# Kernel optimization log

Measured on AMD Instinct MI355X. Metric: run time of the kernel, lower is better.

Reference implementation:

```python
import jax, jax.numpy as jnp
import numpy as np

B, S, E, H, M, Q = 2, 2048, 768, 12, 768, 4
D = E // H  # head_dim = 64
EPS = 1e-5


def _layernorm(x, g, b):
    m = jnp.mean(x, axis=-1, keepdims=True)
    v = jnp.mean((x - m) ** 2, axis=-1, keepdims=True)
    return (x - m) / jnp.sqrt(v + EPS) * g + b


def setup_inputs() -> dict:
    key = jax.random.key(0)
    ks = jax.random.split(key, 12)
    w = lambda k, shape, s=0.02: (jax.random.normal(k, shape) * s).astype(jnp.float32)
    return {
        "x": jax.random.normal(ks[0], (B, S, E), dtype=jnp.float32),
        "ln1_g": jnp.ones((E,), jnp.float32), "ln1_b": jnp.zeros((E,), jnp.float32),
        "wq": w(ks[1], (E, E)), "bq": jnp.zeros((E,), jnp.float32),
        "wk": w(ks[2], (E, E)), "bk": jnp.zeros((E,), jnp.float32),
        "wv": w(ks[3], (E, E)), "bv": jnp.zeros((E,), jnp.float32),
        "wo": w(ks[4], (E, E)), "bo": jnp.zeros((E,), jnp.float32),
        "ln2_g": jnp.ones((E,), jnp.float32), "ln2_b": jnp.zeros((E,), jnp.float32),
        "w1": w(ks[5], (E, Q * M)), "b1": jnp.zeros((Q * M,), jnp.float32),
        "wvqc": w(ks[6], (M, M)), "bvqc": jnp.zeros((M,), jnp.float32),
        "w2": w(ks[7], (Q * M, E)), "b2": jnp.zeros((E,), jnp.float32),
    }


def reference(x, ln1_g, ln1_b, wq, bq, wk, bk, wv, bv, wo, bo,
              ln2_g, ln2_b, w1, b1, wvqc, bvqc, w2, b2):
    b, s, e = x.shape
    h, d = H, e // H

    # --- attention branch (pre-norm, per-query-L2-normalized logits) ---
    xn = _layernorm(x, ln1_g, ln1_b)
    q = (xn @ wq + bq).reshape(b, s, h, d).transpose(0, 2, 1, 3)  # bhsd
    k = (xn @ wk + bk).reshape(b, s, h, d).transpose(0, 2, 1, 3)
    v = (xn @ wv + bv).reshape(b, s, h, d).transpose(0, 2, 1, 3)

    qk = jnp.einsum('bhsd,bhtd->bhst', q, k)                       # [B,H,S,S]
    q_norm2 = jnp.clip(jnp.sum(q * q, axis=-1, keepdims=True), 1e-5)  # [B,H,S,1]
    logits = qk / jnp.sqrt(d * q_norm2)
    attn = jax.nn.softmax(logits, axis=-1)
    vals = jnp.einsum('bhst,bhtd->bhsd', attn, v)
    vals = vals.transpose(0, 2, 1, 3).reshape(b, s, e)
    x = x + (vals @ wo + bo)  # residual; attn dropout is identity in eval

    # --- quantum-style FeedForward with overlapping q_stride slices ---
    xn2 = _layernorm(x, ln2_g, ln2_b)
    hmid = xn2 @ w1 + b1                                           # [B,S,Q*M]
    m = wvqc.shape[0]
    qstride = w1.shape[1] // m
    # overlapping slices h[..., i:i+M] for i in 0..Q-1, stacked on a new axis
    sl = jnp.stack([hmid[..., i:i + m] for i in range(qstride)], axis=2)  # [B,S,Q,M]
    hv = sl @ wvqc + bvqc                                          # vqc linear
    hv = hv.transpose(0, 1, 3, 2).reshape(b, s, qstride * m)       # interleave
    hv = jax.nn.gelu(hv, approximate=False)
    out = x + (hv @ w2 + b2)
    return out
```

## Files before the change

kernel.cpp:

```cpp
#include <hip/hip_runtime.h>
#include <hip/hip_bf16.h>
#include <math.h>

typedef unsigned short ushort_t;
typedef __attribute__((ext_vector_type(8))) short short8;
typedef __attribute__((ext_vector_type(8))) __bf16 bf16x8;
typedef __attribute__((ext_vector_type(4))) float f32x4;
typedef __attribute__((ext_vector_type(4))) unsigned u32x4;

#define SDIM 2048
#define EDIM 768
#define NTOK 4096

static __device__ __forceinline__ ushort_t f2bf(float f) {
  unsigned u = __builtin_bit_cast(unsigned, f);
  u += 0x7fff + ((u >> 16) & 1);
  return (ushort_t)(u >> 16);
}
static __device__ __forceinline__ float bf2f(ushort_t h) {
  return __builtin_bit_cast(float, (unsigned)h << 16);
}
static __device__ __forceinline__ f32x4 mfma16(short8 a, short8 b, f32x4 c) {
  return __builtin_amdgcn_mfma_f32_16x16x32_bf16(
      __builtin_bit_cast(bf16x8, a), __builtin_bit_cast(bf16x8, b), c, 0, 0, 0);
}
static __device__ __forceinline__ void gload_lds16(const void* g, void* l) {
  __builtin_amdgcn_global_load_lds(
      (const __attribute__((address_space(1))) void*)g,
      (__attribute__((address_space(3))) void*)l, 16, 0, 0);
}
static __device__ __forceinline__ unsigned cvtpk(float lo, float hi) {
  unsigned r;
  asm("v_cvt_pk_bf16_f32 %0, %1, %2" : "=v"(r) : "v"(lo), "v"(hi));
  return r;
}

__global__ void k_castT5(const float* __restrict__ wq, const float* __restrict__ wk,
                         const float* __restrict__ wv, const float* __restrict__ wo,
                         const float* __restrict__ wvqc, ushort_t* __restrict__ oqkv,
                         ushort_t* __restrict__ owo, ushort_t* __restrict__ ovqc) {
  __shared__ float tile[32][33];
  const int z = blockIdx.z;
  const float* in = z == 0 ? wq : z == 1 ? wk : z == 2 ? wv : z == 3 ? wo : wvqc;
  ushort_t* out = z < 3 ? oqkv + (size_t)z * 768 * 768 : (z == 3 ? owo : ovqc);
  int c0 = blockIdx.x * 32, r0 = blockIdx.y * 32;
  int tx = threadIdx.x, ty = threadIdx.y;
#pragma unroll
  for (int i = 0; i < 32; i += 8)
    tile[ty + i][tx] = in[(size_t)(r0 + ty + i) * 768 + c0 + tx];
  __syncthreads();
#pragma unroll
  for (int i = 0; i < 32; i += 8)
    out[(size_t)(c0 + ty + i) * 768 + r0 + tx] = f2bf(tile[tx][ty + i]);
}

__global__ void k_castT(const float* __restrict__ in, ushort_t* __restrict__ out,
                        int R, int C) {
  __shared__ float tile[32][33];
  int c0 = blockIdx.x * 32, r0 = blockIdx.y * 32;
  int tx = threadIdx.x, ty = threadIdx.y;
#pragma unroll
  for (int i = 0; i < 32; i += 8)
    tile[ty + i][tx] = in[(size_t)(r0 + ty + i) * C + c0 + tx];
  __syncthreads();
#pragma unroll
  for (int i = 0; i < 32; i += 8)
    out[(size_t)(c0 + ty + i) * R + r0 + tx] = f2bf(tile[tx][ty + i]);
}

__global__ void k_vT(const ushort_t* __restrict__ in, ushort_t* __restrict__ out) {
  __shared__ ushort_t tile[32][34];
  int bh = blockIdx.z;
  int t0 = blockIdx.x * 32, d0 = blockIdx.y * 32;
  const ushort_t* ib = in + (size_t)bh * SDIM * 64;
  ushort_t* ob = out + (size_t)bh * 64 * SDIM;
  int tx = threadIdx.x, ty = threadIdx.y;
#pragma unroll
  for (int i = 0; i < 32; i += 8)
    tile[ty + i][tx] = ib[(size_t)(t0 + ty + i) * 64 + d0 + tx];
  __syncthreads();
  const int T = t0 + tx, tb = T & ~63, tl = T & 63;
  const int tperm =
      tb + 32 * (tl >> 5) + 8 * ((tl >> 2) & 3) + 4 * ((tl >> 4) & 1) + (tl & 3);
#pragma unroll
  for (int i = 0; i < 32; i += 8)
    ob[(size_t)(d0 + ty + i) * SDIM + tperm] = tile[tx][ty + i];
}

__global__ void k_w1shift(const float* __restrict__ w1, ushort_t* __restrict__ w1s) {
  int idx = blockIdx.x * 256 + threadIdx.x;
  int e = idx / 768, m = idx - (idx / 768) * 768;
#pragma unroll
  for (int i = 0; i < 4; i++)
    w1s[((size_t)i * 768 + e) * 768 + m] = f2bf(w1[(size_t)e * 3072 + i + m]);
}

__global__ __launch_bounds__(256) void k_b1eff(const float* __restrict__ b1,
                                               const ushort_t* __restrict__ wvqcT,
                                               const float* __restrict__ bvqc,
                                               float* __restrict__ b1e) {
  const int n = blockIdx.x;
  const int i = n & 3, j = n >> 2;
  const int t = threadIdx.x;
  float s = 0.f;
  for (int m = t; m < 768; m += 256)
    s += b1[i + m] * bf2f(wvqcT[(size_t)j * 768 + m]);
#pragma unroll
  for (int mm = 32; mm; mm >>= 1) s += __shfl_xor(s, mm);
  __shared__ float red[4];
  if ((t & 63) == 0) red[t >> 6] = s;
  __syncthreads();
  if (t == 0) b1e[n] = red[0] + red[1] + red[2] + red[3] + bvqc[j];
}

__global__ __launch_bounds__(256) void k_ln(const float* __restrict__ x,
                                            const float* __restrict__ gam,
                                            const float* __restrict__ bet,
                                            ushort_t* __restrict__ out) {
  const int row = blockIdx.x, t = threadIdx.x;
  const float* xr = x + (size_t)row * EDIM;
  float v0 = xr[t], v1 = xr[t + 256], v2 = xr[t + 512];
  float s = v0 + v1 + v2;
  float s2 = v0 * v0 + v1 * v1 + v2 * v2;
#pragma unroll
  for (int m = 32; m; m >>= 1) { s += __shfl_xor(s, m); s2 += __shfl_xor(s2, m); }
  __shared__ float red[8];
  const int wid = t >> 6, lane = t & 63;
  if (lane == 0) { red[wid] = s; red[4 + wid] = s2; }
  __syncthreads();
  s = red[0] + red[1] + red[2] + red[3];
  s2 = red[4] + red[5] + red[6] + red[7];
  float mean = s * (1.f / EDIM);
  float var = s2 * (1.f / EDIM) - mean * mean;
  float rstd = rsqrtf(var + 1e-5f);
  ushort_t* orow = out + (size_t)row * EDIM;
  orow[t] = f2bf((v0 - mean) * rstd * gam[t] + bet[t]);
  orow[t + 256] = f2bf((v1 - mean) * rstd * gam[t + 256] + bet[t + 256]);
  orow[t + 512] = f2bf((v2 - mean) * rstd * gam[t + 512] + bet[t + 512]);
}

__global__ __launch_bounds__(256) void k_qscale(const ushort_t* __restrict__ q,
                                                float* __restrict__ qs) {
  const int lane = threadIdx.x & 63, w = threadIdx.x >> 6;
  const int row = blockIdx.x * 4 + w;
  float v = bf2f(q[(size_t)row * 64 + lane]);
  float s = v * v;
#pragma unroll
  for (int m = 32; m; m >>= 1) s += __shfl_xor(s, m);
  if (lane == 0) qs[row] = rsqrtf(64.f * fmaxf(s, 1e-5f));
}

template <int MODE, int BM, int BN>
__global__ __launch_bounds__(256) void k_gemm(
    const ushort_t* __restrict__ A, const ushort_t* __restrict__ Bt, int lda,
    int ldb, int kc, const float* __restrict__ b0, const float* __restrict__ b1p,
    const float* __restrict__ b2p, float* __restrict__ outF,
    const float* __restrict__ resid, ushort_t* __restrict__ o0,
    ushort_t* __restrict__ o1, ushort_t* __restrict__ o2, int ldc) {
  constexpr int MT = BM / 32, NT = BN / 32;
  constexpr int NPA = BM / 32, NPB = BN / 32;
  __shared__ ushort_t As[2][BM * 64];
  __shared__ ushort_t Bs[2][BN * 64];
  const int t = threadIdx.x;
  const int m0 = blockIdx.x * BM, n0 = blockIdx.y * BN;
  if (MODE == 3) Bt += (size_t)blockIdx.z * 768 * 768;
  const int rowa = t >> 3;
  const int gseg = ((t & 7) ^ (rowa & 7)) * 8;
  const ushort_t* ga = A + (size_t)(m0 + rowa) * lda + gseg;
  const ushort_t* gb = Bt + (size_t)(n0 + rowa) * ldb + gseg;
  const int ldst = t * 8;
  const int lane = t & 63, wid = t >> 6;
  const int g = lane >> 4, c = lane & 15;
  const int wm = (wid >> 1) * (BM / 2), wn = (wid & 1) * (BN / 2);
  const int swz = (c & 7) * 8;
  f32x4 acc[MT][NT] = {};

#define STAGE(BUF, K0)                                                           \
  {                                                                              \
    _Pragma("unroll") for (int p = 0; p < NPA; p++)                              \
        gload_lds16(ga + (K0) + (size_t)(p * 32) * lda, As[BUF] + p * 2048 + ldst);\
    _Pragma("unroll") for (int p = 0; p < NPB; p++)                              \
        gload_lds16(gb + (K0) + (size_t)(p * 32) * ldb, Bs[BUF] + p * 2048 + ldst);\
  }

  STAGE(0, 0);
  __syncthreads();
  int cur = 0;
  for (int k0 = 0; k0 < kc; k0 += 64) {
    if (k0 + 64 < kc) STAGE(cur ^ 1, k0 + 64);
    short8 af[2][MT], bfr[2][NT];
#pragma unroll
    for (int kk = 0; kk < 2; kk++) {
#pragma unroll
      for (int mt = 0; mt < MT; mt++)
        af[kk][mt] = *(const short8*)(As[cur] + (wm + mt * 16 + c) * 64 +
                                      ((g * 8 + kk * 32) ^ swz));
#pragma unroll
      for (int nt = 0; nt < NT; nt++)
        bfr[kk][nt] = *(const short8*)(Bs[cur] + (wn + nt * 16 + c) * 64 +
                                       ((g * 8 + kk * 32) ^ swz));
    }
    __builtin_amdgcn_s_setprio(1);
#pragma unroll
    for (int kk = 0; kk < 2; kk++)
#pragma unroll
      for (int mt = 0; mt < MT; mt++)
#pragma unroll
        for (int nt = 0; nt < NT; nt++)
          acc[mt][nt] = mfma16(af[kk][mt], bfr[kk][nt], acc[mt][nt]);
    __builtin_amdgcn_s_setprio(0);
    __syncthreads();
    cur ^= 1;
  }
#undef STAGE

#pragma unroll
  for (int mt = 0; mt < MT; mt++) {
#pragma unroll
    for (int nt = 0; nt < NT; nt++) {
#pragma unroll
      for (int r = 0; r < 4; r++) {
        int row = m0 + wm + mt * 16 + g * 4 + r;
        int col = n0 + wn + nt * 16 + c;
        float val = acc[mt][nt][r];
        if constexpr (MODE == 0) {
          int which = col / 768;
          int nn = col - which * 768;
          int h = nn >> 6, d = nn & 63;
          int bb = row >> 11, s = row & 2047;
          const float* bp = which == 0 ? b0 : (which == 1 ? b1p : b2p);
          ushort_t* dp = which == 0 ? o0 : (which == 1 ? o1 : o2);
          dp[(((size_t)(bb * 12 + h)) * SDIM + s) * 64 + d] = f2bf(val + bp[nn]);
        } else if constexpr (MODE == 1) {
          size_t o = (size_t)row * ldc + col;
          outF[o] = resid[o] + val + b0[col];
        } else if constexpr (MODE == 2) {
          float xg = val + b0[col];
          float z2 = xg * (1.5957691216f + 0.0713548162f * xg * xg);
          float ge = xg / (1.f + __expf(-z2));
          o0[(size_t)row * ldc + col] = f2bf(ge);
        } else {
          o0[((size_t)row * 4 + blockIdx.z) * ldc + col] = f2bf(val);
        }
      }
    }
  }
}

__global__ __launch_bounds__(256) void k_attn(const ushort_t* __restrict__ q,
                                              const ushort_t* __restrict__ k,
                                              const ushort_t* __restrict__ vt,
                                              const float* __restrict__ qs,
                                              ushort_t* __restrict__ vals) {
  const int tid = threadIdx.x;
  const int wid = tid >> 6, lane = tid & 63;
  const int g = lane >> 4, c = lane & 15;
  const int bh = blockIdx.y;
  const int q0 = blockIdx.x * 64 + wid * 16;
  const int bb = bh / 12, h = bh - bb * 12;
  const ushort_t* qb = q + (size_t)bh * SDIM * 64;
  const ushort_t* kb = k + (size_t)bh * SDIM * 64;
  const ushort_t* vb = vt + (size_t)bh * 64 * SDIM;

  __shared__ ushort_t Ks[2][64 * 64];
  __shared__ ushort_t Vs[2][64 * 64];

  const float scq = qs[bh * SDIM + q0 + c];
  short8 a0 = *(const short8*)(qb + (size_t)(q0 + c) * 64 + g * 8);
  short8 a1 = *(const short8*)(qb + (size_t)(q0 + c) * 64 + 32 + g * 8);
  short8 bq0, bq1;
#pragma unroll
  for (int j = 0; j < 8; j++) {
    bq0[j] = (short)f2bf(bf2f((ushort_t)a0[j]) * scq);
    bq1[j] = (short)f2bf(bf2f((ushort_t)a1[j]) * scq);
  }

  const int srow = tid >> 3, sj = tid & 7;

#define STAGE(BUF, T0)                                                          \
  {                                                                             \
    _Pragma("unroll") for (int n = 0; n < 2; n++) {                             \
      const int row = n * 32 + srow;                                            \
      const int scol = (sj ^ (row & 7)) * 8;                                    \
      gload_lds16(kb + (size_t)((T0) + row) * 64 + scol,                        \
                  Ks[BUF] + n * 2048 + tid * 8);                                \
      gload_lds16(vb + (size_t)row * SDIM + (T0) + scol,                        \
                  Vs[BUF] + n * 2048 + tid * 8);                                \
    }                                                                           \
  }

  f32x4 accO[4] = {};
  float mr = 0.f, ls = 0.f;
  const int sw = (c & 7) << 4;

  STAGE(0, 0);
  __syncthreads();
  int cur = 0;
  for (int t0 = 0; t0 < SDIM; t0 += 64) {
    if (t0 + 64 < SDIM) STAGE(cur ^ 1, t0 + 64);
    const char* Kc = (const char*)Ks[cur];
    const char* Vc = (const char*)Vs[cur];
    f32x4 s[4] = {};
    __builtin_amdgcn_s_setprio(1);
#pragma unroll
    for (int i = 0; i < 4; i++) {
      const int rb = (i * 16 + c) * 128;
      short8 ka0 = *(const short8*)(Kc + rb + ((g * 16) ^ sw));
      short8 ka1 = *(const short8*)(Kc + rb + ((64 + g * 16) ^ sw));
      s[i] = mfma16(ka0, bq0, s[i]);
      s[i] = mfma16(ka1, bq1, s[i]);
    }
    __builtin_amdgcn_s_setprio(0);
    float pm = s[0][0];
#pragma unroll
    for (int i = 0; i < 4; i++)
#pragma unroll
      for (int r = 0; r < 4; r++) pm = fmaxf(pm, s[i][r]);
    pm = fmaxf(pm, __shfl_xor(pm, 16));
    pm = fmaxf(pm, __shfl_xor(pm, 32));
    if (__any(pm - mr > 8.f)) {
      float nm = fmaxf(mr, pm);
      float al = __expf(mr - nm);
      ls *= al;
      mr = nm;
#pragma unroll
      for (int r = 0; r < 4; r++) {
        float alr = __shfl(al, (lane & 0x30) | ((lane >> 4) * 4 + r));
#pragma unroll
        for (int dt = 0; dt < 4; dt++) accO[dt][r] *= alr;
      }
    }
    float p[4][4];
#pragma unroll
    for (int i = 0; i < 4; i++)
#pragma unroll
      for (int r = 0; r < 4; r++) {
        p[i][r] = __expf(s[i][r] - mr);
        ls += p[i][r];
      }
    u32x4 w0 = {cvtpk(p[0][0], p[0][1]), cvtpk(p[0][2], p[0][3]),
                cvtpk(p[1][0], p[1][1]), cvtpk(p[1][2], p[1][3])};
    u32x4 w1 = {cvtpk(p[2][0], p[2][1]), cvtpk(p[2][2], p[2][3]),
                cvtpk(p[3][0], p[3][1]), cvtpk(p[3][2], p[3][3])};
    short8 pa0 = __builtin_bit_cast(short8, w0);
    short8 pa1 = __builtin_bit_cast(short8, w1);
    __builtin_amdgcn_s_setprio(1);
#pragma unroll
    for (int dt = 0; dt < 4; dt++) {
      const int vbse = (dt * 16 + c) * 128;
      short8 v0 = *(const short8*)(Vc + vbse + ((g * 16) ^ sw));
      short8 v1 = *(const short8*)(Vc + vbse + ((64 + g * 16) ^ sw));
      accO[dt] = mfma16(pa0, v0, accO[dt]);
      accO[dt] = mfma16(pa1, v1, accO[dt]);
    }
    __builtin_amdgcn_s_setprio(0);
    __syncthreads();
    cur ^= 1;
  }
#undef STAGE

  ls += __shfl_xor(ls, 16);
  ls += __shfl_xor(ls, 32);
  float inv = 1.f / ls;
  float invr[4];
#pragma unroll
  for (int r = 0; r < 4; r++)
    invr[r] = __shfl(inv, (lane & 0x30) | ((lane >> 4) * 4 + r));
#pragma unroll
  for (int dt = 0; dt < 4; dt++)
#pragma unroll
    for (int r = 0; r < 4; r++) {
      int s = q0 + 4 * g + r;
      float val = accO[dt][r] * invr[r];
      vals[((size_t)(bb * SDIM + s)) * EDIM + h * 64 + dt * 16 + c] = f2bf(val);
    }
}

extern "C" void kernel_launch(void* const* d_in, const int* in_sizes, int n_in,
                              void* d_out, int out_size, void* d_ws, size_t ws_size,
                              hipStream_t stream) {
  const float* x = (const float*)d_in[0];
  const float* ln1g = (const float*)d_in[1];
  const float* ln1b = (const float*)d_in[2];
  const float* wq = (const float*)d_in[3];
  const float* bq = (const float*)d_in[4];
  const float* wk = (const float*)d_in[5];
  const float* bk = (const float*)d_in[6];
  const float* wv = (const float*)d_in[7];
  const float* bv = (const float*)d_in[8];
  const float* wo = (const float*)d_in[9];
  const float* bo = (const float*)d_in[10];
  const float* ln2g = (const float*)d_in[11];
  const float* ln2b = (const float*)d_in[12];
  const float* w1 = (const float*)d_in[13];
  const float* b1 = (const float*)d_in[14];
  const float* wvqc = (const float*)d_in[15];
  const float* bvqc = (const float*)d_in[16];
  const float* w2 = (const float*)d_in[17];
  const float* b2 = (const float*)d_in[18];
  float* out = (float*)d_out;

  char* w = (char*)d_ws;
  ushort_t* xn = (ushort_t*)(w + 0);
  ushort_t* vtb = (ushort_t*)(w + 0);
  ushort_t* xn2 = (ushort_t*)(w + 6291456);
  float* x2 = (float*)(w + 12582912);
  ushort_t* qb = (ushort_t*)(w + 25165824);
  ushort_t* kb = (ushort_t*)(w + 31457280);
  ushort_t* vb = (ushort_t*)(w + 37748736);
  ushort_t* vals = (ushort_t*)(w + 44040192);
  ushort_t* G = (ushort_t*)(w + 25165824);
  float* qsc = (float*)(w + 50331648);
  ushort_t* wqkvT = (ushort_t*)(w + 50528256);
  ushort_t* woT = (ushort_t*)(w + 54067200);
  ushort_t* wvqcT = (ushort_t*)(w + 55246848);
  ushort_t* w1s = (ushort_t*)(w + 56426496);
  ushort_t* W1eT = (ushort_t*)(w + 61145088);
  float* b1e = (float*)(w + 65863680);
  ushort_t* w2T = (ushort_t*)(w + 65875968);

  dim3 tb(32, 8);
  k_castT5<<<dim3(24, 24, 5), tb, 0, stream>>>(wq, wk, wv, wo, wvqc, wqkvT, woT,
                                               wvqcT);
  k_castT<<<dim3(24, 96), tb, 0, stream>>>(w2, w2T, 3072, 768);
  k_w1shift<<<2304, 256, 0, stream>>>(w1, w1s);
  k_b1eff<<<3072, 256, 0, stream>>>(b1, wvqcT, bvqc, b1e);
  k_gemm<3, 128, 128><<<dim3(6, 6, 4), 256, 0, stream>>>(
      wvqcT, w1s, 768, 768, 768, nullptr, nullptr, nullptr, nullptr, nullptr,
      W1eT, nullptr, nullptr, 768);
  k_ln<<<4096, 256, 0, stream>>>(x, ln1g, ln1b, xn);
  k_gemm<0, 128, 128><<<dim3(32, 18), 256, 0, stream>>>(
      xn, wqkvT, 768, 768, 768, bq, bk, bv, nullptr, nullptr, qb, kb, vb, 0);
  k_vT<<<dim3(64, 2, 24), tb, 0, stream>>>(vb, vtb);
  k_qscale<<<12288, 256, 0, stream>>>(qb, qsc);
  k_attn<<<dim3(32, 24), 256, 0, stream>>>(qb, kb, vtb, qsc, vals);
  k_gemm<1, 64, 64><<<dim3(64, 12), 256, 0, stream>>>(
      vals, woT, 768, 768, 768, bo, nullptr, nullptr, x2, x, nullptr, nullptr,
      nullptr, 768);
  k_ln<<<4096, 256, 0, stream>>>(x2, ln2g, ln2b, xn2);
  k_gemm<2, 128, 128><<<dim3(32, 24), 256, 0, stream>>>(
      xn2, W1eT, 768, 768, 768, b1e, nullptr, nullptr, nullptr, nullptr, G,
      nullptr, nullptr, 3072);
  k_gemm<1, 64, 64><<<dim3(64, 12), 256, 0, stream>>>(
      G, w2T, 3072, 3072, 3072, b2, nullptr, nullptr, out, x2, nullptr, nullptr,
      nullptr, 768);
}
```

Before: 222.0 us.

## Rework attention softmax: exp2 with folded log2e, MFMA row-sum, max3 reduction

Result: no change. 217.7 us (-2.0%).

```diff
diff --git a/kernel.cpp b/kernel.cpp
--- a/kernel.cpp
+++ b/kernel.cpp
@@ -32,6 +32,20 @@
 static __device__ __forceinline__ unsigned cvtpk(float lo, float hi) {
   unsigned r;
   asm("v_cvt_pk_bf16_f32 %0, %1, %2" : "=v"(r) : "v"(lo), "v"(hi));
+  return r;
+}
+static __device__ __forceinline__ float exp2fast(float x) {
+#if __has_builtin(__builtin_amdgcn_exp2f)
+  return __builtin_amdgcn_exp2f(x);
+#else
+  float r;
+  asm("v_exp_f32 %0, %1" : "=v"(r) : "v"(x));
+  return r;
+#endif
+}
+static __device__ __forceinline__ float max3f(float a, float b, float c) {
+  float r;
+  asm("v_max3_f32 %0, %1, %2, %3" : "=v"(r) : "v"(a), "v"(b), "v"(c));
   return r;
 }
 
@@ -265,7 +279,7 @@
   __shared__ ushort_t Ks[2][64 * 64];
   __shared__ ushort_t Vs[2][64 * 64];
 
-  const float scq = qs[bh * SDIM + q0 + c];
+  const float scq = qs[bh * SDIM + q0 + c] * 1.44269504089f;
   short8 a0 = *(const short8*)(qb + (size_t)(q0 + c) * 64 + g * 8);
   short8 a1 = *(const short8*)(qb + (size_t)(q0 + c) * 64 + 32 + g * 8);
   short8 bq0, bq1;
@@ -274,6 +288,8 @@
     bq0[j] = (short)f2bf(bf2f((ushort_t)a0[j]) * scq);
     bq1[j] = (short)f2bf(bf2f((ushort_t)a1[j]) * scq);
   }
+  const short8 ones = {0x3F80, 0x3F80, 0x3F80, 0x3F80,
+                       0x3F80, 0x3F80, 0x3F80, 0x3F80};
 
   const int srow = tid >> 3, sj = tid & 7;
 
@@ -290,7 +306,9 @@
   }
 
   f32x4 accO[4] = {};
-  float mr = 0.f, ls = 0.f;
+  f32x4 accL = {};
+  float mr = 0.f;
+  float negmr = 0.f;
   const int sw = (c & 7) << 4;
 
   STAGE(0, 0);
@@ -300,7 +318,9 @@
     if (t0 + 64 < SDIM) STAGE(cur ^ 1, t0 + 64);
     const char* Kc = (const char*)Ks[cur];
     const char* Vc = (const char*)Vs[cur];
-    f32x4 s[4] = {};
+    f32x4 s[4];
+#pragma unroll
+    for (int i = 0; i < 4; i++) s[i] = {negmr, negmr, negmr, negmr};
     __builtin_amdgcn_s_setprio(1);
 #pragma unroll
     for (int i = 0; i < 4; i++) {
@@ -311,40 +331,46 @@
       s[i] = mfma16(ka1, bq1, s[i]);
     }
     __builtin_amdgcn_s_setprio(0);
-    float pm = s[0][0];
-#pragma unroll
-    for (int i = 0; i < 4; i++)
-#pragma unroll
-      for (int r = 0; r < 4; r++) pm = fmaxf(pm, s[i][r]);
-    pm = fmaxf(pm, __shfl_xor(pm, 16));
-    pm = fmaxf(pm, __shfl_xor(pm, 32));
-    if (__any(pm - mr > 8.f)) {
-      float nm = fmaxf(mr, pm);
-      float al = __expf(mr - nm);
-      ls *= al;
-      mr = nm;
+    float pm = max3f(s[0][0], s[0][1], s[0][2]);
+    pm = max3f(pm, s[0][3], s[1][0]);
+    pm = max3f(pm, s[1][1], s[1][2]);
+    pm = max3f(pm, s[1][3], s[2][0]);
+    pm = max3f(pm, s[2][1], s[2][2]);
+    pm = max3f(pm, s[2][3], s[3][0]);
+    pm = max3f(pm, s[3][1], s[3][2]);
+    pm = fmaxf(pm, s[3][3]);
+    if (__any(pm > 12.f)) {
+      pm = fmaxf(pm, __shfl_xor(pm, 16));
+      pm = fmaxf(pm, __shfl_xor(pm, 32));
+      float delta = fmaxf(pm, 0.f);
+      mr += delta;
+      negmr = -mr;
+      float al = exp2fast(-delta);
+#pragma unroll
+      for (int i = 0; i < 4; i++)
+#pragma unroll
+        for (int r = 0; r < 4; r++) s[i][r] -= delta;
 #pragma unroll
       for (int r = 0; r < 4; r++) {
         float alr = __shfl(al, (lane & 0x30) | ((lane >> 4) * 4 + r));
 #pragma unroll
         for (int dt = 0; dt < 4; dt++) accO[dt][r] *= alr;
+        accL[r] *= alr;
       }
     }
-    float p[4][4];
-#pragma unroll
-    for (int i = 0; i < 4; i++)
-#pragma unroll
-      for (int r = 0; r < 4; r++) {
-        p[i][r] = __expf(s[i][r] - mr);
-        ls += p[i][r];
-      }
-    u32x4 w0 = {cvtpk(p[0][0], p[0][1]), cvtpk(p[0][2], p[0][3]),
-                cvtpk(p[1][0], p[1][1]), cvtpk(p[1][2], p[1][3])};
-    u32x4 w1 = {cvtpk(p[2][0], p[2][1]), cvtpk(p[2][2], p[2][3]),
-                cvtpk(p[3][0], p[3][1]), cvtpk(p[3][2], p[3][3])};
+    u32x4 w0 = {cvtpk(exp2fast(s[0][0]), exp2fast(s[0][1])),
+                cvtpk(exp2fast(s[0][2]), exp2fast(s[0][3])),
+                cvtpk(exp2fast(s[1][0]), exp2fast(s[1][1])),
+                cvtpk(exp2fast(s[1][2]), exp2fast(s[1][3]))};
+    u32x4 w1 = {cvtpk(exp2fast(s[2][0]), exp2fast(s[2][1])),
+                cvtpk(exp2fast(s[2][2]), exp2fast(s[2][3])),
+                cvtpk(exp2fast(s[3][0]), exp2fast(s[3][1])),
+                cvtpk(exp2fast(s[3][2]), exp2fast(s[3][3]))};
     short8 pa0 = __builtin_bit_cast(short8, w0);
     short8 pa1 = __builtin_bit_cast(short8, w1);
     __builtin_amdgcn_s_setprio(1);
+    accL = mfma16(pa0, ones, accL);
+    accL = mfma16(pa1, ones, accL);
 #pragma unroll
     for (int dt = 0; dt < 4; dt++) {
       const int vbse = (dt * 16 + c) * 128;
@@ -359,13 +385,9 @@
   }
 #undef STAGE
 
-  ls += __shfl_xor(ls, 16);
-  ls += __shfl_xor(ls, 32);
-  float inv = 1.f / ls;
   float invr[4];
 #pragma unroll
-  for (int r = 0; r < 4; r++)
-    invr[r] = __shfl(inv, (lane & 0x30) | ((lane >> 4) * 4 + r));
+  for (int r = 0; r < 4; r++) invr[r] = 1.f / accL[r];
 #pragma unroll
   for (int dt = 0; dt < 4; dt++)
 #pragma unroll
```
